# Kernel tuning notes

Hardware: AMD Instinct MI355X
Metric: run time of the kernel (lower is better)

## Reference

```python
import jax, jax.numpy as jnp
import numpy as np

DIM = 768
B, N = 16, 1024
EPS_LN = 1e-5

def _layernorm(x, gamma, beta):
    mu = jnp.mean(x, axis=-1, keepdims=True)
    var = jnp.mean((x - mu) ** 2, axis=-1, keepdims=True)
    return (x - mu) * jax.lax.rsqrt(var + EPS_LN) * gamma + beta

def _gelu(x):
    return jax.nn.gelu(x, approximate=False)

def setup_inputs() -> dict:
    key = jax.random.key(0)
    ks = jax.random.split(key, 10)
    d = DIM
    s1 = 1.0 / np.sqrt(2 * d)
    s = 1.0 / np.sqrt(d)
    return {
        "x": jax.random.normal(ks[0], (B, N, d), dtype=jnp.float32),
        "gamma": jnp.ones((d,), jnp.float32),
        "beta": jnp.zeros((d,), jnp.float32),
        "w1": jax.random.normal(ks[1], (2 * d, d), jnp.float32) * s1,
        "b1": jnp.zeros((d,), jnp.float32),
        "w2": jax.random.normal(ks[2], (d, d), jnp.float32) * s,
        "b2": jnp.zeros((d,), jnp.float32),
        "w3": jax.random.normal(ks[3], (d, d), jnp.float32) * s,
        "b3": jnp.zeros((d,), jnp.float32),
        "w4": jax.random.normal(ks[4], (d, d), jnp.float32) * s,
        "b4": jnp.zeros((d,), jnp.float32),
    }

def reference(x, gamma, beta, w1, b1, w2, b2, w3, b3, w4, b4):
    # x: [B, N, D]
    avg_x = jnp.mean(x, axis=1)                      # [B, D]
    A = avg_x[:, None, :] * jax.nn.sigmoid(_layernorm(x, gamma, beta))  # [B, N, D]
    # batched pairwise Euclidean distance among tokens (replaces python loop)
    sq = jnp.sum(A * A, axis=-1)                     # [B, N]
    d2 = sq[:, :, None] + sq[:, None, :] - 2.0 * jnp.einsum('bnd,bmd->bnm', A, A)
    dist = jnp.sqrt(jnp.clip(d2, 1e-12))             # [B, N, N]
    m = jnp.max(dist, axis=-1)                       # [B, N]
    m_x = x + m[..., None]                           # [B, N, D]
    cat = jnp.concatenate([A, m_x], axis=-1)         # [B, N, 2D]
    m1 = _gelu(cat @ w1 + b1)                        # layer1
    W = _gelu(m1 @ w2 + b2)                          # layer2
    Wdyn = x * W
    l3 = _gelu((m1 * Wdyn) @ w3 + b3)                # layer3
    out = _gelu((x * l3) @ w4 + b4)                  # layer4
    return out.astype(jnp.float32)
```

## Files before the change

kernel.cpp:

```cpp
#include <hip/hip_runtime.h>
#include <hip/hip_fp16.h>
#include <math.h>

#define DIM 768
#define NTOK 1024
#define NBATCH 16
#define BNR (NBATCH * NTOK)

typedef _Float16 f16x8 __attribute__((ext_vector_type(8)));
typedef float f32x4 __attribute__((ext_vector_type(4)));

__device__ __forceinline__ void gl2lds16(const void* g, void* l) {
    __builtin_amdgcn_global_load_lds(
        (const __attribute__((address_space(1))) void*)g,
        (__attribute__((address_space(3))) void*)l, 16, 0, 0);
}

__device__ __forceinline__ float gelu_fast(float z) {
    const float s = z * 0.70710678118654752f;
    const float ax = fabsf(s);
    const float t = __builtin_amdgcn_rcpf(1.0f + 0.3275911f * ax);
    const float poly = t * (0.254829592f + t * (-0.284496736f +
                       t * (1.421413741f + t * (-1.453152027f + t * 1.061405429f))));
    const float e = __expf(-ax * ax);
    float erfv = 1.0f - poly * e;
    erfv = copysignf(erfv, s);
    return 0.5f * z * (1.0f + erfv);
}

__device__ __forceinline__ float us2f(unsigned short u) {
    __half_raw hr; hr.x = u; return __half2float(__half(hr));
}

__global__ __launch_bounds__(256) void avg_kernel(const float* __restrict__ x,
                                                  float* __restrict__ avgx) {
    const int d = blockIdx.x * 256 + threadIdx.x;
    const int b = blockIdx.y;
    const int n0 = blockIdx.z * 128;
    const float* xp = x + (size_t)b * NTOK * DIM + (size_t)n0 * DIM + d;
    float s = 0.0f;
    for (int n = 0; n < 128; ++n) s += xp[(size_t)n * DIM];
    atomicAdd(&avgx[b * DIM + d], s * (1.0f / NTOK));
}

__global__ __launch_bounds__(256) void colsum_w1b(const float* __restrict__ w1,
                                                  float* __restrict__ s1) {
    const int col = blockIdx.x * 256 + threadIdx.x;
    const int r0 = 768 + blockIdx.y * 64;
    float s = 0.0f;
    #pragma unroll 8
    for (int r = 0; r < 64; ++r) s += w1[(size_t)(r0 + r) * 768 + col];
    atomicAdd(&s1[col], s);
}

__global__ __launch_bounds__(256) void ln_sig_kernel(
    const float* __restrict__ x, const float* __restrict__ gamma,
    const float* __restrict__ beta, const float* __restrict__ avgx,
    __half* __restrict__ Ah, __half* __restrict__ xh, float* __restrict__ sq)
{
    const int wv = threadIdx.x >> 6, lane = threadIdx.x & 63;
    const int row = blockIdx.x * 4 + wv;
    const int b = row >> 10;
    const float* xr = x + (size_t)row * DIM;
    float4 v[3];
    #pragma unroll
    for (int i = 0; i < 3; ++i) v[i] = *(const float4*)&xr[i * 256 + lane * 4];
    float s = v[0].x + v[0].y + v[0].z + v[0].w
            + v[1].x + v[1].y + v[1].z + v[1].w
            + v[2].x + v[2].y + v[2].z + v[2].w;
    #pragma unroll
    for (int o = 32; o > 0; o >>= 1) s += __shfl_xor(s, o, 64);
    const float mu = s * (1.0f / DIM);
    float ss = 0.0f;
    #pragma unroll
    for (int i = 0; i < 3; ++i) {
        const float dx0 = v[i].x - mu, dx1 = v[i].y - mu, dx2 = v[i].z - mu, dx3 = v[i].w - mu;
        ss += dx0 * dx0 + dx1 * dx1 + dx2 * dx2 + dx3 * dx3;
    }
    #pragma unroll
    for (int o = 32; o > 0; o >>= 1) ss += __shfl_xor(ss, o, 64);
    const float rstd = rsqrtf(ss * (1.0f / DIM) + 1e-5f);
    float qs = 0.0f;
    #pragma unroll
    for (int i = 0; i < 3; ++i) {
        const int d0 = i * 256 + lane * 4;
        const float4 g4 = *(const float4*)&gamma[d0];
        const float4 b4 = *(const float4*)&beta[d0];
        const float4 a4 = *(const float4*)&avgx[b * DIM + d0];
        ushort4 pa, px;
        const float xv[4] = {v[i].x, v[i].y, v[i].z, v[i].w};
        const float gv[4] = {g4.x, g4.y, g4.z, g4.w};
        const float bv[4] = {b4.x, b4.y, b4.z, b4.w};
        const float av[4] = {a4.x, a4.y, a4.z, a4.w};
        unsigned short pav[4], pxv[4];
        #pragma unroll
        for (int j = 0; j < 4; ++j) {
            const float ln = (xv[j] - mu) * rstd * gv[j] + bv[j];
            const float sg = 1.0f / (1.0f + expf(-ln));
            const float a = av[j] * sg;
            const __half h = __float2half(a);
            const float ar = __half2float(h);
            qs += ar * ar;
            pav[j] = __half_as_ushort(h);
            pxv[j] = __half_as_ushort(__float2half(xv[j]));
        }
        pa.x = pav[0]; pa.y = pav[1]; pa.z = pav[2]; pa.w = pav[3];
        px.x = pxv[0]; px.y = pxv[1]; px.z = pxv[2]; px.w = pxv[3];
        *(ushort4*)&Ah[(size_t)row * DIM + d0] = pa;
        *(ushort4*)&xh[(size_t)row * DIM + d0] = px;
    }
    #pragma unroll
    for (int o = 32; o > 0; o >>= 1) qs += __shfl_xor(qs, o, 64);
    if (lane == 0) sq[row] = qs;
}

__device__ __forceinline__ void wconv_body(const float* __restrict__ w,
                                           __half* __restrict__ wT, int K, int N,
                                           int bx, int by)
{
    __shared__ float t[64][65];
    const int k0 = by * 64, n0 = bx * 64;
    const int tid = threadIdx.x;
    const int r = tid >> 4, c4 = (tid & 15) * 4;
    #pragma unroll
    for (int p = 0; p < 4; ++p) {
        const int rr = p * 16 + r;
        const float4 v = *(const float4*)&w[(size_t)(k0 + rr) * N + n0 + c4];
        t[rr][c4] = v.x; t[rr][c4 + 1] = v.y; t[rr][c4 + 2] = v.z; t[rr][c4 + 3] = v.w;
    }
    __syncthreads();
    #pragma unroll
    for (int p = 0; p < 4; ++p) {
        const int nn = p * 16 + r;
        ushort4 pk;
        pk.x = __half_as_ushort(__float2half(t[c4 + 0][nn]));
        pk.y = __half_as_ushort(__float2half(t[c4 + 1][nn]));
        pk.z = __half_as_ushort(__float2half(t[c4 + 2][nn]));
        pk.w = __half_as_ushort(__float2half(t[c4 + 3][nn]));
        *(ushort4*)&wT[(size_t)(n0 + nn) * K + k0 + c4] = pk;
    }
}

__global__ __launch_bounds__(256) void wconv(const float* __restrict__ w,
                                             __half* __restrict__ wT, int K, int N)
{
    wconv_body(w, wT, K, N, blockIdx.x, blockIdx.y);
}

__global__ __launch_bounds__(256) void wconv3(const float* __restrict__ w2,
                                              const float* __restrict__ w3,
                                              const float* __restrict__ w4,
                                              __half* __restrict__ t2,
                                              __half* __restrict__ t3,
                                              __half* __restrict__ t4)
{
    const float* w = (blockIdx.z == 0) ? w2 : (blockIdx.z == 1) ? w3 : w4;
    __half* wT = (blockIdx.z == 0) ? t2 : (blockIdx.z == 1) ? t3 : t4;
    wconv_body(w, wT, 768, 768, blockIdx.x, blockIdx.y);
}

template<int K, bool CAT, int EPI>
__global__ __launch_bounds__(512, 2) void gemm256(
    const __half* __restrict__ A0, const __half* __restrict__ A1,
    const __half* __restrict__ BT, const float* __restrict__ bias,
    const float* __restrict__ xin, const __half* __restrict__ m1h,
    const float* __restrict__ mv, const float* __restrict__ sv,
    __half* __restrict__ outH, float* __restrict__ outF)
{
    __shared__ _Float16 As[2][256 * 64];
    __shared__ _Float16 Bs[2][192 * 64];
    const int tid = threadIdx.x;
    const int w = tid >> 6, lane = tid & 63;
    const int wu = __builtin_amdgcn_readfirstlane(w);
    const int wr = w >> 1, wc = w & 1;
    const int R0 = blockIdx.x * 256, J0 = blockIdx.y * 192;
    constexpr int rs = CAT ? DIM : K;
    const int srow = lane >> 3;
    const int soct = ((lane & 7) ^ ((lane >> 3) & 7)) * 8;
    constexpr int NT = K / 64;

    f32x4 acc[4][6];
    #pragma unroll
    for (int mt = 0; mt < 4; ++mt)
        #pragma unroll
        for (int nt = 0; nt < 6; ++nt) {
            f32x4 z = {0.0f, 0.0f, 0.0f, 0.0f};
            acc[mt][nt] = z;
        }

    auto stage = [&](int buf, int k0) {
        const __half* Ab = (CAT && k0 >= DIM) ? (A1 + (k0 - DIM)) : (A0 + k0);
        #pragma unroll
        for (int o = 0; o < 4; ++o) {
            const int r = o * 64 + w * 8 + srow;
            const int ru = o * 64 + wu * 8;
            gl2lds16(Ab + (size_t)(R0 + r) * rs + soct, &As[buf][ru * 64]);
        }
        #pragma unroll
        for (int o = 0; o < 3; ++o) {
            const int r = o * 64 + w * 8 + srow;
            const int ru = o * 64 + wu * 8;
            gl2lds16(BT + (size_t)(J0 + r) * K + k0 + soct, &Bs[buf][ru * 64]);
        }
    };

    stage(0, 0);
    __syncthreads();
    #pragma unroll 2
    for (int kt = 0; kt < NT; ++kt) {
        const int cur = kt & 1;
        if (kt + 1 < NT) stage(cur ^ 1, (kt + 1) * 64);
        #pragma unroll
        for (int kh = 0; kh < 2; ++kh) {
            f16x8 af[4], bf[6];
            #pragma unroll
            for (int mt = 0; mt < 4; ++mt) {
                const int row = wr * 64 + mt * 16 + (lane & 15);
                const int oct = (kh * 4 + (lane >> 4)) ^ (row & 7);
                af[mt] = *(const f16x8*)&As[cur][row * 64 + oct * 8];
            }
            #pragma unroll
            for (int nt = 0; nt < 6; ++nt) {
                const int row = wc * 96 + nt * 16 + (lane & 15);
                const int oct = (kh * 4 + (lane >> 4)) ^ (row & 7);
                bf[nt] = *(const f16x8*)&Bs[cur][row * 64 + oct * 8];
            }
            #pragma unroll
            for (int mt = 0; mt < 4; ++mt)
                #pragma unroll
                for (int nt = 0; nt < 6; ++nt)
                    acc[mt][nt] = __builtin_amdgcn_mfma_f32_16x16x32_f16(bf[nt], af[mt], acc[mt][nt], 0, 0, 0);
        }
        __syncthreads();
    }

    #pragma unroll
    for (int mt = 0; mt < 4; ++mt) {
        const int row = R0 + wr * 64 + mt * 16 + (lane & 15);
        float mrow = 0.0f;
        if constexpr (EPI == 0) mrow = mv[row];
        #pragma unroll
        for (int nt = 0; nt < 6; ++nt) {
            const int c0 = J0 + wc * 96 + nt * 16 + (lane >> 4) * 4;
            const size_t off = (size_t)row * DIM + c0;
            const float4 b4 = *(const float4*)&bias[c0];
            float g[4];
            if constexpr (EPI == 0) {
                const float4 s4 = *(const float4*)&sv[c0];
                g[0] = gelu_fast(acc[mt][nt][0] + b4.x + mrow * s4.x);
                g[1] = gelu_fast(acc[mt][nt][1] + b4.y + mrow * s4.y);
                g[2] = gelu_fast(acc[mt][nt][2] + b4.z + mrow * s4.z);
                g[3] = gelu_fast(acc[mt][nt][3] + b4.w + mrow * s4.w);
            } else {
                g[0] = gelu_fast(acc[mt][nt][0] + b4.x);
                g[1] = gelu_fast(acc[mt][nt][1] + b4.y);
                g[2] = gelu_fast(acc[mt][nt][2] + b4.z);
                g[3] = gelu_fast(acc[mt][nt][3] + b4.w);
            }
            if constexpr (EPI == 3) {
                float4 o; o.x = g[0]; o.y = g[1]; o.z = g[2]; o.w = g[3];
                *(float4*)&outF[off] = o;
            } else {
                float v[4];
                if constexpr (EPI == 0) {
                    v[0] = g[0]; v[1] = g[1]; v[2] = g[2]; v[3] = g[3];
                } else if constexpr (EPI == 1) {
                    const ushort4 mh = *(const ushort4*)&m1h[off];
                    const float4 x4 = *(const float4*)&xin[off];
                    v[0] = us2f(mh.x) * x4.x * g[0];
                    v[1] = us2f(mh.y) * x4.y * g[1];
                    v[2] = us2f(mh.z) * x4.z * g[2];
                    v[3] = us2f(mh.w) * x4.w * g[3];
                } else {
                    const float4 x4 = *(const float4*)&xin[off];
                    v[0] = x4.x * g[0]; v[1] = x4.y * g[1];
                    v[2] = x4.z * g[2]; v[3] = x4.w * g[3];
                }
                ushort4 pk;
                pk.x = __half_as_ushort(__float2half(v[0]));
                pk.y = __half_as_ushort(__float2half(v[1]));
                pk.z = __half_as_ushort(__float2half(v[2]));
                pk.w = __half_as_ushort(__float2half(v[3]));
                *(ushort4*)&outH[off] = pk;
            }
        }
    }
}

__global__ __launch_bounds__(256, 4) void dist16(const __half* __restrict__ Ah,
                                                 const float* __restrict__ sq,
                                                 float* __restrict__ m)
{
    __shared__ _Float16 As[2][128 * 32];
    __shared__ _Float16 Bs[2][128 * 32];
    const int tid = threadIdx.x;
    const int w = tid >> 6, lane = tid & 63;
    const int wu = __builtin_amdgcn_readfirstlane(w);
    const int wr = w >> 1, wc = w & 1;
    const int base = blockIdx.x * NTOK;
    int t = blockIdx.y, ty = 0;
    while (t >= 8 - ty) { t -= 8 - ty; ++ty; }
    const int tz = ty + t;
    const int I0 = ty * 128, J0 = tz * 128;
    const int srow = lane >> 2;
    const int sk8 = (((lane & 3) ^ ((lane >> 3) & 3))) * 8;
    const int fx = ((lane >> 4) ^ ((lane >> 1) & 3)) * 8;
    constexpr int NT = DIM / 32;

    f32x4 acc[4][4];
    #pragma unroll
    for (int mt = 0; mt < 4; ++mt)
        #pragma unroll
        for (int nt = 0; nt < 4; ++nt) {
            f32x4 z = {0.0f, 0.0f, 0.0f, 0.0f};
            acc[mt][nt] = z;
        }

    auto stage = [&](int buf, int k0) {
        #pragma unroll
        for (int i = 0; i < 2; ++i) {
            const int rbase = i * 64 + w * 16;
            const int rbu = i * 64 + wu * 16;
            gl2lds16(Ah + (size_t)(base + I0 + rbase + srow) * DIM + k0 + sk8, &As[buf][rbu * 32]);
            gl2lds16(Ah + (size_t)(base + J0 + rbase + srow) * DIM + k0 + sk8, &Bs[buf][rbu * 32]);
        }
    };

    stage(0, 0);
    __syncthreads();
    #pragma unroll 2
    for (int kt = 0; kt < NT; ++kt) {
        const int cur = kt & 1;
        if (kt + 1 < NT) stage(cur ^ 1, (kt + 1) * 32);
        f16x8 af[4], bf[4];
        #pragma unroll
        for (int mt = 0; mt < 4; ++mt)
            af[mt] = *(const f16x8*)&As[cur][(wr * 64 + mt * 16 + (lane & 15)) * 32 + fx];
        #pragma unroll
        for (int nt = 0; nt < 4; ++nt)
            bf[nt] = *(const f16x8*)&Bs[cur][(wc * 64 + nt * 16 + (lane & 15)) * 32 + fx];
        #pragma unroll
        for (int mt = 0; mt < 4; ++mt)
            #pragma unroll
            for (int nt = 0; nt < 4; ++nt)
                acc[mt][nt] = __builtin_amdgcn_mfma_f32_16x16x32_f16(af[mt], bf[nt], acc[mt][nt], 0, 0, 0);
        __syncthreads();
    }

    float sqiA[4][4];
    #pragma unroll
    for (int mt = 0; mt < 4; ++mt)
        #pragma unroll
        for (int r = 0; r < 4; ++r)
            sqiA[mt][r] = sq[base + I0 + wr * 64 + mt * 16 + (lane >> 4) * 4 + r];
    float sqjA[4];
    #pragma unroll
    for (int nt = 0; nt < 4; ++nt)
        sqjA[nt] = sq[base + J0 + wc * 64 + nt * 16 + (lane & 15)];

    #pragma unroll
    for (int mt = 0; mt < 4; ++mt) {
        float vmax[4] = {-1e30f, -1e30f, -1e30f, -1e30f};
        #pragma unroll
        for (int nt = 0; nt < 4; ++nt)
            #pragma unroll
            for (int r = 0; r < 4; ++r)
                vmax[r] = fmaxf(vmax[r], sqiA[mt][r] + sqjA[nt] - 2.0f * acc[mt][nt][r]);
        #pragma unroll
        for (int r = 0; r < 4; ++r) {
            float v = vmax[r];
            v = fmaxf(v, __shfl_xor(v, 1, 64));
            v = fmaxf(v, __shfl_xor(v, 2, 64));
            v = fmaxf(v, __shfl_xor(v, 4, 64));
            v = fmaxf(v, __shfl_xor(v, 8, 64));
            if ((lane & 15) == 0) {
                const float d = sqrtf(fmaxf(v, 1e-12f));
                atomicMax((unsigned int*)&m[base + I0 + wr * 64 + mt * 16 + (lane >> 4) * 4 + r],
                          __float_as_uint(d));
            }
        }
    }

    if (I0 != J0) {
        #pragma unroll
        for (int nt = 0; nt < 4; ++nt) {
            float cm = -1e30f;
            #pragma unroll
            for (int mt = 0; mt < 4; ++mt)
                #pragma unroll
                for (int r = 0; r < 4; ++r)
                    cm = fmaxf(cm, sqiA[mt][r] + sqjA[nt] - 2.0f * acc[mt][nt][r]);
            cm = fmaxf(cm, __shfl_xor(cm, 16, 64));
            cm = fmaxf(cm, __shfl_xor(cm, 32, 64));
            if ((lane >> 4) == 0) {
                const float d = sqrtf(fmaxf(cm, 1e-12f));
                atomicMax((unsigned int*)&m[base + J0 + wc * 64 + nt * 16 + (lane & 15)],
                          __float_as_uint(d));
            }
        }
    }
}

extern "C" void kernel_launch(void* const* d_in, const int* in_sizes, int n_in,
                              void* d_out, int out_size, void* d_ws, size_t ws_size,
                              hipStream_t stream)
{
    const float* x     = (const float*)d_in[0];
    const float* gamma = (const float*)d_in[1];
    const float* beta  = (const float*)d_in[2];
    const float* w1    = (const float*)d_in[3];
    const float* b1    = (const float*)d_in[4];
    const float* w2    = (const float*)d_in[5];
    const float* b2    = (const float*)d_in[6];
    const float* w3    = (const float*)d_in[7];
    const float* b3    = (const float*)d_in[8];
    const float* w4    = (const float*)d_in[9];
    const float* b4    = (const float*)d_in[10];
    float* out = (float*)d_out;
    float* ws  = (float*)d_ws;

    float* avgx = ws;
    float* mbuf = ws + 12288;
    float* s1   = mbuf + 16384;
    float* sq   = s1 + 768;
    __half* w1T = (__half*)(sq + 16384);
    __half* w2T = w1T + (size_t)1536 * 768;
    __half* w3T = w2T + (size_t)768 * 768;
    __half* w4T = w3T + (size_t)768 * 768;
    __half* P0  = w4T + (size_t)768 * 768;
    __half* P1  = P0 + (size_t)BNR * DIM;
    __half* Ah  = (__half*)d_out;
    __half* xh  = Ah + (size_t)BNR * DIM;

    hipMemsetAsync(ws, 0, (12288 + 16384 + 768) * sizeof(float), stream);
    wconv<<<dim3(12, 24), 256, 0, stream>>>(w1, w1T, 1536, 768);
    wconv3<<<dim3(12, 12, 3), 256, 0, stream>>>(w2, w3, w4, w2T, w3T, w4T);
    colsum_w1b<<<dim3(3, 12), 256, 0, stream>>>(w1, s1);
    avg_kernel<<<dim3(3, NBATCH, 8), 256, 0, stream>>>(x, avgx);
    ln_sig_kernel<<<BNR / 4, 256, 0, stream>>>(x, gamma, beta, avgx, Ah, xh, sq);
    dist16<<<dim3(NBATCH, 36), 256, 0, stream>>>(Ah, sq, mbuf);
    gemm256<1536, true, 0><<<dim3(64, 4), 512, 0, stream>>>(
        Ah, xh, w1T, b1, nullptr, nullptr, mbuf, s1, P0, nullptr);
    gemm256<768, false, 1><<<dim3(64, 4), 512, 0, stream>>>(
        P0, nullptr, w2T, b2, x, P0, nullptr, nullptr, P1, nullptr);
    gemm256<768, false, 2><<<dim3(64, 4), 512, 0, stream>>>(
        P1, nullptr, w3T, b3, x, nullptr, nullptr, nullptr, P0, nullptr);
    gemm256<768, false, 3><<<dim3(64, 4), 512, 0, stream>>>(
        P0, nullptr, w4T, b4, x, nullptr, nullptr, nullptr, nullptr, out);
}
```

Measured before the change: 326.8 us.

## Rework GEMM into 3-stage LDS ring with 2x4 warp layout and ping-pong barriers

```diff
diff --git a/kernel.cpp b/kernel.cpp
--- a/kernel.cpp
+++ b/kernel.cpp
@@ -160,88 +160,126 @@
 }
 
 template<int K, bool CAT, int EPI>
-__global__ __launch_bounds__(512, 2) void gemm256(
+__global__ __launch_bounds__(512, 2) void gemm8p(
     const __half* __restrict__ A0, const __half* __restrict__ A1,
     const __half* __restrict__ BT, const float* __restrict__ bias,
     const float* __restrict__ xin, const __half* __restrict__ m1h,
     const float* __restrict__ mv, const float* __restrict__ sv,
     __half* __restrict__ outH, float* __restrict__ outF)
 {
-    __shared__ _Float16 As[2][256 * 64];
-    __shared__ _Float16 Bs[2][192 * 64];
+    __shared__ _Float16 As[3][256 * 32];
+    __shared__ _Float16 Bs[3][192 * 32];
     const int tid = threadIdx.x;
     const int w = tid >> 6, lane = tid & 63;
     const int wu = __builtin_amdgcn_readfirstlane(w);
-    const int wr = w >> 1, wc = w & 1;
+    const int wr = w >> 2, wc = w & 3;
     const int R0 = blockIdx.x * 256, J0 = blockIdx.y * 192;
     constexpr int rs = CAT ? DIM : K;
-    const int srow = lane >> 3;
-    const int soct = ((lane & 7) ^ ((lane >> 3) & 7)) * 8;
-    constexpr int NT = K / 64;
-
-    f32x4 acc[4][6];
-    #pragma unroll
-    for (int mt = 0; mt < 4; ++mt)
-        #pragma unroll
-        for (int nt = 0; nt < 6; ++nt) {
+    const int srow = lane >> 2;
+    const int sk8 = (((lane & 3) ^ ((lane >> 3) & 3))) * 8;
+    const int fx = ((lane >> 4) ^ ((lane >> 1) & 3)) * 8;
+    constexpr int NT = K / 32;
+    static_assert(NT % 3 == 0, "3-buffer ring needs NT % 3 == 0");
+
+    f32x4 acc[8][3];
+    #pragma unroll
+    for (int mt = 0; mt < 8; ++mt)
+        #pragma unroll
+        for (int nt = 0; nt < 3; ++nt) {
             f32x4 z = {0.0f, 0.0f, 0.0f, 0.0f};
             acc[mt][nt] = z;
         }
 
-    auto stage = [&](int buf, int k0) {
+    auto stage = [&](int buf, int kt2) {
+        const int k0 = kt2 * 32;
         const __half* Ab = (CAT && k0 >= DIM) ? (A1 + (k0 - DIM)) : (A0 + k0);
         #pragma unroll
-        for (int o = 0; o < 4; ++o) {
-            const int r = o * 64 + w * 8 + srow;
-            const int ru = o * 64 + wu * 8;
-            gl2lds16(Ab + (size_t)(R0 + r) * rs + soct, &As[buf][ru * 64]);
-        }
-        #pragma unroll
-        for (int o = 0; o < 3; ++o) {
-            const int r = o * 64 + w * 8 + srow;
-            const int ru = o * 64 + wu * 8;
-            gl2lds16(BT + (size_t)(J0 + r) * K + k0 + soct, &Bs[buf][ru * 64]);
+        for (int i = 0; i < 3; ++i) {
+            const int s = wu + 8 * i;
+            if (s < 16)
+                gl2lds16(Ab + (size_t)(R0 + s * 16 + srow) * rs + sk8,
+                         &As[buf][(s * 16) * 32]);
+            else
+                gl2lds16(BT + (size_t)(J0 + (s - 16) * 16 + srow) * K + k0 + sk8,
+                         &Bs[buf][((s - 16) * 16) * 32]);
+        }
+        if (wu < 4) {
+            const int s = wu + 24;
+            gl2lds16(BT + (size_t)(J0 + (s - 16) * 16 + srow) * K + k0 + sk8,
+                     &Bs[buf][((s - 16) * 16) * 32]);
         }
     };
 
     stage(0, 0);
-    __syncthreads();
-    #pragma unroll 2
+    stage(1, 1);
+    if (wu < 4) { asm volatile("s_waitcnt vmcnt(4)" ::: "memory"); }
+    else        { asm volatile("s_waitcnt vmcnt(3)" ::: "memory"); }
+    asm volatile("s_barrier" ::: "memory");
+
+    #pragma unroll 3
     for (int kt = 0; kt < NT; ++kt) {
-        const int cur = kt & 1;
-        if (kt + 1 < NT) stage(cur ^ 1, (kt + 1) * 64);
-        #pragma unroll
-        for (int kh = 0; kh < 2; ++kh) {
-            f16x8 af[4], bf[6];
+        const int cur = kt % 3;
+        {
+            f16x8 af[4], bf[3];
             #pragma unroll
             for (int mt = 0; mt < 4; ++mt) {
-                const int row = wr * 64 + mt * 16 + (lane & 15);
-                const int oct = (kh * 4 + (lane >> 4)) ^ (row & 7);
-                af[mt] = *(const f16x8*)&As[cur][row * 64 + oct * 8];
-            }
-            #pragma unroll
-            for (int nt = 0; nt < 6; ++nt) {
-                const int row = wc * 96 + nt * 16 + (lane & 15);
-                const int oct = (kh * 4 + (lane >> 4)) ^ (row & 7);
-                bf[nt] = *(const f16x8*)&Bs[cur][row * 64 + oct * 8];
-            }
+                const int row = wr * 128 + mt * 16 + (lane & 15);
+                af[mt] = *(const f16x8*)&As[cur][row * 32 + fx];
+            }
+            #pragma unroll
+            for (int nt = 0; nt < 3; ++nt) {
+                const int row = wc * 48 + nt * 16 + (lane & 15);
+                bf[nt] = *(const f16x8*)&Bs[cur][row * 32 + fx];
+            }
+            if (kt + 2 < NT) stage((kt + 2) % 3, kt + 2);
+            asm volatile("s_barrier" ::: "memory");
+            __builtin_amdgcn_s_setprio(1);
             #pragma unroll
             for (int mt = 0; mt < 4; ++mt)
                 #pragma unroll
-                for (int nt = 0; nt < 6; ++nt)
+                for (int nt = 0; nt < 3; ++nt)
                     acc[mt][nt] = __builtin_amdgcn_mfma_f32_16x16x32_f16(bf[nt], af[mt], acc[mt][nt], 0, 0, 0);
-        }
-        __syncthreads();
-    }
-
-    #pragma unroll
-    for (int mt = 0; mt < 4; ++mt) {
-        const int row = R0 + wr * 64 + mt * 16 + (lane & 15);
+            __builtin_amdgcn_s_setprio(0);
+            asm volatile("s_barrier" ::: "memory");
+        }
+        {
+            f16x8 af[4], bf[3];
+            #pragma unroll
+            for (int mt = 0; mt < 4; ++mt) {
+                const int row = wr * 128 + 64 + mt * 16 + (lane & 15);
+                af[mt] = *(const f16x8*)&As[cur][row * 32 + fx];
+            }
+            #pragma unroll
+            for (int nt = 0; nt < 3; ++nt) {
+                const int row = wc * 48 + nt * 16 + (lane & 15);
+                bf[nt] = *(const f16x8*)&Bs[cur][row * 32 + fx];
+            }
+            if (kt + 2 < NT) {
+                if (wu < 4) { asm volatile("s_waitcnt vmcnt(4)" ::: "memory"); }
+                else        { asm volatile("s_waitcnt vmcnt(3)" ::: "memory"); }
+            } else if (kt + 1 < NT) {
+                asm volatile("s_waitcnt vmcnt(0)" ::: "memory");
+            }
+            asm volatile("s_barrier" ::: "memory");
+            __builtin_amdgcn_s_setprio(1);
+            #pragma unroll
+            for (int mt = 0; mt < 4; ++mt)
+                #pragma unroll
+                for (int nt = 0; nt < 3; ++nt)
+                    acc[4 + mt][nt] = __builtin_amdgcn_mfma_f32_16x16x32_f16(bf[nt], af[mt], acc[4 + mt][nt], 0, 0, 0);
+            __builtin_amdgcn_s_setprio(0);
+            asm volatile("s_barrier" ::: "memory");
+        }
+    }
+
+    #pragma unroll
+    for (int mt = 0; mt < 8; ++mt) {
+        const int row = R0 + wr * 128 + mt * 16 + (lane & 15);
         float mrow = 0.0f;
         if constexpr (EPI == 0) mrow = mv[row];
         #pragma unroll
-        for (int nt = 0; nt < 6; ++nt) {
-            const int c0 = J0 + wc * 96 + nt * 16 + (lane >> 4) * 4;
+        for (int nt = 0; nt < 3; ++nt) {
+            const int c0 = J0 + wc * 48 + nt * 16 + (lane >> 4) * 4;
             const size_t off = (size_t)row * DIM + c0;
             const float4 b4 = *(const float4*)&bias[c0];
             float g[4];
@@ -439,12 +477,12 @@
     avg_kernel<<<dim3(3, NBATCH, 8), 256, 0, stream>>>(x, avgx);
     ln_sig_kernel<<<BNR / 4, 256, 0, stream>>>(x, gamma, beta, avgx, Ah, xh, sq);
     dist16<<<dim3(NBATCH, 36), 256, 0, stream>>>(Ah, sq, mbuf);
-    gemm256<1536, true, 0><<<dim3(64, 4), 512, 0, stream>>>(
+    gemm8p<1536, true, 0><<<dim3(64, 4), 512, 0, stream>>>(
         Ah, xh, w1T, b1, nullptr, nullptr, mbuf, s1, P0, nullptr);
-    gemm256<768, false, 1><<<dim3(64, 4), 512, 0, stream>>>(
+    gemm8p<768, false, 1><<<dim3(64, 4), 512, 0, stream>>>(
         P0, nullptr, w2T, b2, x, P0, nullptr, nullptr, P1, nullptr);
-    gemm256<768, false, 2><<<dim3(64, 4), 512, 0, stream>>>(
+    gemm8p<768, false, 2><<<dim3(64, 4), 512, 0, stream>>>(
         P1, nullptr, w3T, b3, x, nullptr, nullptr, nullptr, P0, nullptr);
-    gemm256<768, false, 3><<<dim3(64, 4), 512, 0, stream>>>(
+    gemm8p<768, false, 3><<<dim3(64, 4), 512, 0, stream>>>(
         P0, nullptr, w4T, b4, x, nullptr, nullptr, nullptr, nullptr, out);
 }
```

After: 333.0 us. Within noise of the previous version (+1.9%).
